# Optimization experiments

Measured on AMD Instinct MI355X. Metric: run time of the kernel, lower is better.

The kernel has to match this reference:

```python
import jax, jax.numpy as jnp
import numpy as np

POOLED = 7      # pooled_size
KSIZE = 2       # kernel_size (max-pool window & stride)
CROP = POOLED * KSIZE  # crop_and_resize crop_size = 14


def setup_inputs() -> dict:
    key = jax.random.key(0)
    k1, k2 = jax.random.split(key)
    feature_maps = jax.random.normal(k1, (2, 50, 50, 512), dtype=jnp.float32)
    # normalized boxes in [x1, y1, x2, y2] order (the layer swaps to y1,x1,y2,x2);
    # tf.image.crop_and_resize handles arbitrary (even inverted) boxes, so raw
    # uniforms are valid inputs.
    rois = jax.random.uniform(k2, (2, 128, 4), dtype=jnp.float32)
    return {"feature_maps": feature_maps, "rois": rois}


def _roi_pool(feature_maps, rois):
    B, H, W, C = feature_maps.shape
    R = rois.shape[1]
    N = B * R
    # [x1,y1,x2,y2] -> [y1,x1,y2,x2] as in the layer
    boxes = rois.reshape(N, 4)[:, jnp.array([1, 0, 3, 2])]
    y1, x1, y2, x2 = boxes[:, 0], boxes[:, 1], boxes[:, 2], boxes[:, 3]
    bidx = jnp.repeat(jnp.arange(B), R)  # box_indices, [N]

    # tf.image.crop_and_resize sample grid (crop_size > 1 branch)
    i = jnp.arange(CROP, dtype=feature_maps.dtype)
    ys = y1[:, None] * (H - 1) + i[None, :] * ((y2 - y1)[:, None] * (H - 1) / (CROP - 1))  # [N,S]
    xs = x1[:, None] * (W - 1) + i[None, :] * ((x2 - x1)[:, None] * (W - 1) / (CROP - 1))  # [N,S]
    valid_y = (ys >= 0) & (ys <= H - 1)
    valid_x = (xs >= 0) & (xs <= W - 1)

    y0f = jnp.floor(ys)
    x0f = jnp.floor(xs)
    wy = (ys - y0f)[:, :, None, None]   # [N,S,1,1]
    wx = (xs - x0f)[:, None, :, None]   # [N,1,S,1]
    y0i = jnp.clip(y0f.astype(jnp.int32), 0, H - 1)
    y1i = jnp.clip(y0i + 1, 0, H - 1)
    x0i = jnp.clip(x0f.astype(jnp.int32), 0, W - 1)
    x1i = jnpp = None
    x1i = jnp.clip(x0i + 1, 0, W - 1)

    # gather the two bilinear rows per sample line: [N, S, W, C]
    rows0 = feature_maps[bidx[:, None], y0i]
    rows1 = feature_maps[bidx[:, None], y1i]
    rows = rows0 + (rows1 - rows0) * wy  # lerp in y

    # gather the two columns and lerp in x: [N, S, S, C]
    v0 = jnp.take_along_axis(rows, x0i[:, None, :, None], axis=2)
    v1 = jnp.take_along_axis(rows, x1i[:, None, :, None], axis=2)
    crops = v0 + (v1 - v0) * wx

    # out-of-range samples -> extrapolation_value = 0 (TF default)
    valid = valid_y[:, :, None, None] & valid_x[:, None, :, None]
    crops = jnp.where(valid, crops, jnp.zeros((), crops.dtype))

    # 2x2/stride-2 max pool -> [N, POOLED, POOLED, C]
    pooled = crops.reshape(N, POOLED, KSIZE, POOLED, KSIZE, C).max(axis=(2, 4))
    return pooled


def reference(feature_maps, rois):
    # flatten=False, keep_batch_dim=False -> [batch*num_rois, pooled, pooled, C]
    return _roi_pool(feature_maps, rois)
```

## Files before the change

### kernel.cpp

```cpp
#include <hip/hip_runtime.h>


constexpr int H = 50, W = 50, C = 512;
constexpr int POOLEDX = 7, KSIZE = 2, CROP = 14;
constexpr int RPB = 128;
constexpr int C4 = C / 4;
constexpr int NXCD = 8;
constexpr int PIX = POOLEDX * POOLEDX;
constexpr int NROI = 2 * RPB;
constexpr int ROIS_PER_XCD = NROI / NXCD;

__global__ __launch_bounds__(C4) void roi_pool_kernel(
    const float* __restrict__ fm,
    const float* __restrict__ rois,
    float* __restrict__ out)
{
    const int hw   = blockIdx.x;
    const int xcd  = hw & (NXCD - 1);
    const int slot = hw >> 3;
    const int n    = xcd * ROIS_PER_XCD + slot / PIX;
    const int k    = slot % PIX;
    const int ph   = k / POOLEDX;
    const int pw   = k % POOLEDX;
    const int b    = n / RPB;
    const int t    = threadIdx.x;

    const float4* __restrict__ fm4 = reinterpret_cast<const float4*>(fm);

    const float x1 = rois[n * 4 + 0];
    const float y1 = rois[n * 4 + 1];
    const float x2 = rois[n * 4 + 2];
    const float y2 = rois[n * 4 + 3];

    const float ybase = y1 * (float)(H - 1);
    const float xbase = x1 * (float)(W - 1);
    const float ystep = (y2 - y1) * (float)(H - 1) / (float)(CROP - 1);
    const float xstep = (x2 - x1) * (float)(W - 1) / (float)(CROP - 1);

    const int fmbase = b * H * W;

    int   x0i[KSIZE], x1i[KSIZE];
    float wx[KSIZE];
    bool  vx[KSIZE];
    #pragma unroll
    for (int kx = 0; kx < KSIZE; ++kx) {
        const int   ix = pw * KSIZE + kx;
        const float xs = xbase + (float)ix * xstep;
        vx[kx] = (xs >= 0.0f) && (xs <= (float)(W - 1));
        const float x0f = floorf(xs);
        wx[kx] = xs - x0f;
        int xi = (int)x0f;
        xi = min(max(xi, 0), W - 1);
        x0i[kx] = xi;
        x1i[kx] = min(xi + 1, W - 1);
    }

    float4 acc;
    acc.x = acc.y = acc.z = acc.w = -__builtin_inff();

    #pragma unroll
    for (int ky = 0; ky < KSIZE; ++ky) {
        const int   iy = ph * KSIZE + ky;
        const float ys = ybase + (float)iy * ystep;
        const bool  vy = (ys >= 0.0f) && (ys <= (float)(H - 1));
        const float y0f = floorf(ys);
        const float wy  = ys - y0f;
        int y0i = (int)y0f;
        y0i = min(max(y0i, 0), H - 1);
        const int y1i = min(y0i + 1, H - 1);

        #pragma unroll
        for (int kx = 0; kx < KSIZE; ++kx) {
            const int p00 = (fmbase + y0i * W + x0i[kx]) * C4 + t;
            const int p01 = (fmbase + y0i * W + x1i[kx]) * C4 + t;
            const int p10 = (fmbase + y1i * W + x0i[kx]) * C4 + t;
            const int p11 = (fmbase + y1i * W + x1i[kx]) * C4 + t;

            const float4 f00 = fm4[p00];
            const float4 f01 = fm4[p01];
            const float4 f10 = fm4[p10];
            const float4 f11 = fm4[p11];

            float4 v;
            {
                const float r0 = f00.x + (f10.x - f00.x) * wy;
                const float r1 = f01.x + (f11.x - f01.x) * wy;
                v.x = r0 + (r1 - r0) * wx[kx];
            }
            {
                const float r0 = f00.y + (f10.y - f00.y) * wy;
                const float r1 = f01.y + (f11.y - f01.y) * wy;
                v.y = r0 + (r1 - r0) * wx[kx];
            }
            {
                const float r0 = f00.z + (f10.z - f00.z) * wy;
                const float r1 = f01.z + (f11.z - f01.z) * wy;
                v.z = r0 + (r1 - r0) * wx[kx];
            }
            {
                const float r0 = f00.w + (f10.w - f00.w) * wy;
                const float r1 = f01.w + (f11.w - f01.w) * wy;
                v.w = r0 + (r1 - r0) * wx[kx];
            }

            const bool valid = vx[kx] && vy;
            if (!valid) { v.x = 0.0f; v.y = 0.0f; v.z = 0.0f; v.w = 0.0f; }

            acc.x = fmaxf(acc.x, v.x);
            acc.y = fmaxf(acc.y, v.y);
            acc.z = fmaxf(acc.z, v.z);
            acc.w = fmaxf(acc.w, v.w);
        }
    }

    float4* __restrict__ out4 = reinterpret_cast<float4*>(out);
    const int oblk = (n * PIX + ph * POOLEDX + pw);
    out4[oblk * C4 + t] = acc;
}

extern "C" void kernel_launch(void* const* d_in, const int* in_sizes, int n_in,
                              void* d_out, int out_size, void* d_ws, size_t ws_size,
                              hipStream_t stream) {
    const float* fm   = (const float*)d_in[0];
    const float* rois = (const float*)d_in[1];
    float* out = (float*)d_out;

    const int nblocks = NROI * PIX;
    roi_pool_kernel<<<nblocks, C4, 0, stream>>>(fm, rois, out);
}
```

Baseline: 82.25 us.

## Convert feature map to fp16 in a pre-pass and gather half-precision corners

Adds a conversion kernel that writes the fp32 feature map into the workspace as fp16 on every call. The ROI-pool kernel then gathers 8 channels per 16-byte load instead of 4, runs 64 threads per block instead of 128, and does the bilinear and max math in fp32. The goal is to halve the bytes moved by the heavily repeated corner gathers. The cost is an extra full read and write pass over the feature map plus a second launch, and rounding inputs to fp16 may loosen accuracy against the fp32 reference.

```diff
diff --git a/kernel.cpp b/kernel.cpp
--- a/kernel.cpp
+++ b/kernel.cpp
@@ -1,17 +1,33 @@
 #include <hip/hip_runtime.h>
+#include <hip/hip_fp16.h>
 
 
 constexpr int H = 50, W = 50, C = 512;
 constexpr int POOLEDX = 7, KSIZE = 2, CROP = 14;
 constexpr int RPB = 128;
-constexpr int C4 = C / 4;
 constexpr int NXCD = 8;
 constexpr int PIX = POOLEDX * POOLEDX;
 constexpr int NROI = 2 * RPB;
 constexpr int ROIS_PER_XCD = NROI / NXCD;
+constexpr int NELEM = 2 * H * W * C;
 
-__global__ __launch_bounds__(C4) void roi_pool_kernel(
-    const float* __restrict__ fm,
+__global__ __launch_bounds__(256) void cvt_kernel(
+    const float* __restrict__ in, __half* __restrict__ out)
+{
+    const int i = (blockIdx.x * 256 + threadIdx.x) * 8;
+    const float4* in4 = reinterpret_cast<const float4*>(in + i);
+    const float4 a = in4[0];
+    const float4 b = in4[1];
+    __half h[8];
+    h[0] = __float2half(a.x); h[1] = __float2half(a.y);
+    h[2] = __float2half(a.z); h[3] = __float2half(a.w);
+    h[4] = __float2half(b.x); h[5] = __float2half(b.y);
+    h[6] = __float2half(b.z); h[7] = __float2half(b.w);
+    *reinterpret_cast<float4*>(out + i) = *reinterpret_cast<const float4*>(h);
+}
+
+__global__ __launch_bounds__(64) void roi_pool_kernel(
+    const __half* __restrict__ fmh,
     const float* __restrict__ rois,
     float* __restrict__ out)
 {
@@ -25,7 +41,7 @@
     const int b    = n / RPB;
     const int t    = threadIdx.x;
 
-    const float4* __restrict__ fm4 = reinterpret_cast<const float4*>(fm);
+    const float4* __restrict__ fm4 = reinterpret_cast<const float4*>(fmh);
 
     const float x1 = rois[n * 4 + 0];
     const float y1 = rois[n * 4 + 1];
@@ -55,8 +71,9 @@
         x1i[kx] = min(xi + 1, W - 1);
     }
 
-    float4 acc;
-    acc.x = acc.y = acc.z = acc.w = -__builtin_inff();
+    float acc[8];
+    #pragma unroll
+    for (int c = 0; c < 8; ++c) acc[c] = -__builtin_inff();
 
     #pragma unroll
     for (int ky = 0; ky < KSIZE; ++ky) {
@@ -71,51 +88,57 @@
 
         #pragma unroll
         for (int kx = 0; kx < KSIZE; ++kx) {
-            const int p00 = (fmbase + y0i * W + x0i[kx]) * C4 + t;
-            const int p01 = (fmbase + y0i * W + x1i[kx]) * C4 + t;
-            const int p10 = (fmbase + y1i * W + x0i[kx]) * C4 + t;
-            const int p11 = (fmbase + y1i * W + x1i[kx]) * C4 + t;
+            const int p00 = (fmbase + y0i * W + x0i[kx]) * (C / 8) + t;
+            const int p01 = (fmbase + y0i * W + x1i[kx]) * (C / 8) + t;
+            const int p10 = (fmbase + y1i * W + x0i[kx]) * (C / 8) + t;
+            const int p11 = (fmbase + y1i * W + x1i[kx]) * (C / 8) + t;
 
-            const float4 f00 = fm4[p00];
-            const float4 f01 = fm4[p01];
-            const float4 f10 = fm4[p10];
-            const float4 f11 = fm4[p11];
+            const float4 r00 = fm4[p00];
+            const float4 r01 = fm4[p01];
+            const float4 r10 = fm4[p10];
+            const float4 r11 = fm4[p11];
 
-            float4 v;
-            {
-                const float r0 = f00.x + (f10.x - f00.x) * wy;
-                const float r1 = f01.x + (f11.x - f01.x) * wy;
-                v.x = r0 + (r1 - r0) * wx[kx];
-            }
-            {
-                const float r0 = f00.y + (f10.y - f00.y) * wy;
-                const float r1 = f01.y + (f11.y - f01.y) * wy;
-                v.y = r0 + (r1 - r0) * wx[kx];
-            }
-            {
-                const float r0 = f00.z + (f10.z - f00.z) * wy;
-                const float r1 = f01.z + (f11.z - f01.z) * wy;
-                v.z = r0 + (r1 - r0) * wx[kx];
-            }
-            {
-                const float r0 = f00.w + (f10.w - f00.w) * wy;
-                const float r1 = f01.w + (f11.w - f01.w) * wy;
-                v.w = r0 + (r1 - r0) * wx[kx];
-            }
+            const __half2* h00 = reinterpret_cast<const __half2*>(&r00);
+            const __half2* h01 = reinterpret_cast<const __half2*>(&r01);
+            const __half2* h10 = reinterpret_cast<const __half2*>(&r10);
+            const __half2* h11 = reinterpret_cast<const __half2*>(&r11);
 
             const bool valid = vx[kx] && vy;
-            if (!valid) { v.x = 0.0f; v.y = 0.0f; v.z = 0.0f; v.w = 0.0f; }
+            const float wxk = wx[kx];
 
-            acc.x = fmaxf(acc.x, v.x);
-            acc.y = fmaxf(acc.y, v.y);
-            acc.z = fmaxf(acc.z, v.z);
-            acc.w = fmaxf(acc.w, v.w);
+            #pragma unroll
+            for (int q = 0; q < 4; ++q) {
+                const float2 f00 = __half22float2(h00[q]);
+                const float2 f01 = __half22float2(h01[q]);
+                const float2 f10 = __half22float2(h10[q]);
+                const float2 f11 = __half22float2(h11[q]);
+
+                float vA, vB;
+                {
+                    const float r0 = f00.x + (f10.x - f00.x) * wy;
+                    const float r1 = f01.x + (f11.x - f01.x) * wy;
+                    vA = r0 + (r1 - r0) * wxk;
+                }
+                {
+                    const float r0 = f00.y + (f10.y - f00.y) * wy;
+                    const float r1 = f01.y + (f11.y - f01.y) * wy;
+                    vB = r0 + (r1 - r0) * wxk;
+                }
+                if (!valid) { vA = 0.0f; vB = 0.0f; }
+                acc[2 * q]     = fmaxf(acc[2 * q],     vA);
+                acc[2 * q + 1] = fmaxf(acc[2 * q + 1], vB);
+            }
         }
     }
 
+    const int oblk = n * PIX + ph * POOLEDX + pw;
     float4* __restrict__ out4 = reinterpret_cast<float4*>(out);
-    const int oblk = (n * PIX + ph * POOLEDX + pw);
-    out4[oblk * C4 + t] = acc;
+    const int obase = oblk * (C / 4) + t * 2;
+    float4 o0, o1;
+    o0.x = acc[0]; o0.y = acc[1]; o0.z = acc[2]; o0.w = acc[3];
+    o1.x = acc[4]; o1.y = acc[5]; o1.z = acc[6]; o1.w = acc[7];
+    out4[obase]     = o0;
+    out4[obase + 1] = o1;
 }
 
 extern "C" void kernel_launch(void* const* d_in, const int* in_sizes, int n_in,
@@ -123,8 +146,11 @@
                               hipStream_t stream) {
     const float* fm   = (const float*)d_in[0];
     const float* rois = (const float*)d_in[1];
-    float* out = (float*)d_out;
+    float* out  = (float*)d_out;
+    __half* fmh = (__half*)d_ws;
+
+    cvt_kernel<<<NELEM / (256 * 8), 256, 0, stream>>>(fm, fmh);
 
     const int nblocks = NROI * PIX;
-    roi_pool_kernel<<<nblocks, C4, 0, stream>>>(fm, rois, out);
+    roi_pool_kernel<<<nblocks, 64, 0, stream>>>(fmh, rois, out);
 }
```

New measurement: 79.94 us. -2.8%, faster.
